# Performance work log

Hardware: AMD Instinct MI355X
Metric: run time of the kernel (lower is better)

## Reference

```python
import jax, jax.numpy as jnp
import numpy as np

B, S, D, H = 4, 2048, 1024, 16
DK = D // H
NEG = -1e9  # stand-in for -inf; keeps softmax grads NaN-free, same math after softmax


def setup_inputs() -> dict:
    key = jax.random.key(0)
    ks = jax.random.split(key, 8)
    scale = 0.02
    return {
        "q": jax.random.normal(ks[0], (B, S, D), jnp.float32),
        "k": jax.random.normal(ks[1], (B, S, D), jnp.float32),
        "v": jax.random.normal(ks[2], (B, S, D), jnp.float32),
        "mask": jnp.ones((B, S), jnp.int32),
        "Wq": jax.random.normal(ks[3], (D, D), jnp.float32) * scale,
        "bq": jnp.zeros((D,), jnp.float32),
        "Wk": jax.random.normal(ks[4], (D, D), jnp.float32) * scale,
        "bk": jnp.zeros((D,), jnp.float32),
        "Wv": jax.random.normal(ks[5], (D, D), jnp.float32) * scale,
        "bv": jnp.zeros((D,), jnp.float32),
        "Wp": jax.random.normal(ks[6], (D, D), jnp.float32) * scale,
        "bp": jnp.zeros((D,), jnp.float32),
    }


def reference(q, k, v, mask, Wq, bq, Wk, bk, Wv, bv, Wp, bp):
    # torch.nn.Linear: y = x @ W.T + b
    Q = q @ Wq.T + bq  # [B,S,D]
    K = k @ Wk.T + bk
    V = v @ Wv.T + bv
    # split heads -> [B,H,S,dk]
    Q = Q.reshape(B, S, H, DK).transpose(0, 2, 1, 3)
    K = K.reshape(B, S, H, DK).transpose(0, 2, 1, 3)
    V = V.reshape(B, S, H, DK).transpose(0, 2, 1, 3)
    Sc = jnp.einsum("bhqd,bhkd->bhqk", Q, K) / jnp.sqrt(jnp.float32(DK))
    # padding mask: [B,1,1,Sk]
    Sc = jnp.where(mask[:, None, None, :] == 0, NEG, Sc)
    # causal mask (tril), as in the registered buffer
    causal = jnp.tril(jnp.ones((S, S), jnp.bool_))
    Sc = jnp.where(causal, Sc, NEG)
    A = jax.nn.softmax(Sc, axis=-1)  # attn_drop with p=0 is identity
    x = jnp.einsum("bhqk,bhkd->bhqd", A, V)
    x = x.transpose(0, 2, 1, 3).reshape(B, S, D)
    return x @ Wp.T + bp
```

## Files before the change

### kernel.cpp

```cpp
#include <hip/hip_runtime.h>
#include <stdint.h>


#define SZB (8192u * 1024u * 2u)
#define WSZ (1024u * 1024u * 2u)
#define NKT 16
#define SLOT 24576

typedef __attribute__((ext_vector_type(8))) short  short8;
typedef __attribute__((ext_vector_type(4))) float  f32x4;

#define MFMA16(a, b, c) __builtin_amdgcn_mfma_f32_16x16x32_bf16(a, b, c, 0, 0, 0)

__device__ __forceinline__ ushort f2bf(float f) {
  uint32_t u = __float_as_uint(f);
  u += 0x7FFF + ((u >> 16) & 1);
  return (ushort)(u >> 16);
}
__device__ __forceinline__ short8 cvt8(float4 a, float4 b) {
  short8 r;
  r[0] = (short)f2bf(a.x); r[1] = (short)f2bf(a.y);
  r[2] = (short)f2bf(a.z); r[3] = (short)f2bf(a.w);
  r[4] = (short)f2bf(b.x); r[5] = (short)f2bf(b.y);
  r[6] = (short)f2bf(b.z); r[7] = (short)f2bf(b.w);
  return r;
}
__device__ __forceinline__ void gl_lds16(const ushort* g, ushort* l) {
  __builtin_amdgcn_global_load_lds(
      (__attribute__((address_space(1))) void*)g,
      (__attribute__((address_space(3))) void*)l, 16, 0, 0);
}

__global__ __launch_bounds__(256) void cvt_w(
    const float* __restrict__ Wq, const float* __restrict__ Wk,
    const float* __restrict__ Wv, const float* __restrict__ Wp,
    ushort* __restrict__ Wqb, ushort* __restrict__ Wkb,
    ushort* __restrict__ Wvb, ushort* __restrict__ Wpb) {
  const int z = blockIdx.y;
  const float* s = (z == 0) ? Wq : (z == 1) ? Wk : (z == 2) ? Wv : Wp;
  ushort* d = (z == 0) ? Wqb : (z == 1) ? Wkb : (z == 2) ? Wvb : Wpb;
  const size_t i = (size_t)(blockIdx.x * 256 + threadIdx.x) * 8;
  *(short8*)&d[i] = cvt8(*(const float4*)&s[i], *(const float4*)&s[i + 4]);
}

__global__ __launch_bounds__(256) void cvt_in(
    const float* __restrict__ q, const float* __restrict__ k,
    const float* __restrict__ v,
    ushort* __restrict__ qb2, ushort* __restrict__ kb2,
    ushort* __restrict__ vb2) {
  const int z = blockIdx.y;
  const float* s = (z == 0) ? q : (z == 1) ? k : v;
  ushort* d = (z == 0) ? qb2 : (z == 1) ? kb2 : vb2;
  const size_t i = (size_t)(blockIdx.x * 256 + threadIdx.x) * 8;
  *(short8*)&d[i] = cvt8(*(const float4*)&s[i], *(const float4*)&s[i + 4]);
}

__device__ __forceinline__ void core8p(
    const ushort* __restrict__ A, const ushort* __restrict__ Wb,
    ushort* lds, int m0, int n0, f32x4 acc[4][4]) {
  const int tid  = threadIdx.x;
  const int w    = tid >> 6;
  const int lane = tid & 63;
  const int quad = lane >> 4;
  const int l16  = lane & 15;
  const int wm   = (w >> 1) * 64;
  const int wn   = (w & 1) * 64;

  const ushort* asrc[4];
  const ushort* bsrc[2];
#pragma unroll
  for (int i = 0; i < 4; ++i) {
    const int c = tid + 512 * i;
    asrc[i] = A + (size_t)(m0 + (c >> 3)) * 1024 + ((c & 7) ^ ((c >> 3) & 7)) * 8;
  }
#pragma unroll
  for (int i = 0; i < 2; ++i) {
    const int c = tid + 512 * i;
    bsrc[i] = Wb + (size_t)(n0 + (c >> 3)) * 1024 + ((c & 7) ^ ((c >> 3) & 7)) * 8;
  }

  auto stage = [&](int j, int s) {
    ushort* base = lds + s * SLOT + w * 512;
#pragma unroll
    for (int i = 0; i < 4; ++i)
      gl_lds16(asrc[i] + j * 64, base + i * 4096);
#pragma unroll
    for (int i = 0; i < 2; ++i)
      gl_lds16(bsrc[i] + j * 64, base + 16384 + i * 4096);
  };

  const int rsw = (l16 & 7) * 8;
  auto compute = [&](int s) {
    const ushort* pA = lds + s * SLOT;
    const ushort* pB = pA + 16384;
    short8 a[4][2], b[4][2];
#pragma unroll
    for (int f = 0; f < 4; ++f)
#pragma unroll
      for (int ks = 0; ks < 2; ++ks) {
        a[f][ks] = *(const short8*)&pA[(wm + f * 16 + l16) * 64 +
                                       ((ks * 32 + quad * 8) ^ rsw)];
        b[f][ks] = *(const short8*)&pB[(wn + f * 16 + l16) * 64 +
                                       ((ks * 32 + quad * 8) ^ rsw)];
      }
    __builtin_amdgcn_s_setprio(1);
#pragma unroll
    for (int i = 0; i < 4; ++i)
#pragma unroll
      for (int j2 = 0; j2 < 4; ++j2) {
        acc[i][j2] = MFMA16(a[i][0], b[j2][0], acc[i][j2]);
        acc[i][j2] = MFMA16(a[i][1], b[j2][1], acc[i][j2]);
      }
    __builtin_amdgcn_s_setprio(0);
  };

  stage(0, 0);
  stage(1, 1);
  int s = 0;
#pragma unroll 1
  for (int j = 0; j < NKT - 1; ++j) {
    asm volatile("s_waitcnt vmcnt(6)" ::: "memory");
    __builtin_amdgcn_s_barrier();
    __builtin_amdgcn_sched_barrier(0);
    if (j < NKT - 2) {
      int s2 = s + 2; if (s2 >= 3) s2 -= 3;
      stage(j + 2, s2);
    }
    compute(s);
    if (++s == 3) s = 0;
  }
  asm volatile("s_waitcnt vmcnt(0)" ::: "memory");
  __builtin_amdgcn_s_barrier();
  __builtin_amdgcn_sched_barrier(0);
  compute(s);
}

__global__ __launch_bounds__(512, 2) void gemm_qkv8(
    const ushort* __restrict__ qb2, const ushort* __restrict__ kb2,
    const ushort* __restrict__ vb2,
    const ushort* __restrict__ Wqb, const ushort* __restrict__ Wkb,
    const ushort* __restrict__ Wvb,
    const float* __restrict__ bq, const float* __restrict__ bk,
    const float* __restrict__ bv,
    ushort* __restrict__ Qb, ushort* __restrict__ Kb, ushort* __restrict__ Vt) {
  __shared__ ushort lds[3 * SLOT];

  const int z = blockIdx.z;
  const ushort* A    = (z == 0) ? qb2 : (z == 1) ? kb2 : vb2;
  const ushort* W    = (z == 0) ? Wqb : (z == 1) ? Wkb : Wvb;
  const float*  bias = (z == 0) ? bq  : (z == 1) ? bk  : bv;

  const int m0 = blockIdx.x * 256;
  const int n0 = blockIdx.y * 128;

  f32x4 acc[4][4] = {};
  core8p(A, W, lds, m0, n0, acc);

  const int tid  = threadIdx.x;
  const int w    = tid >> 6;
  const int lane = tid & 63;
  const int quad = lane >> 4;
  const int l16  = lane & 15;
  const int wm   = (w >> 1) * 64;
  const int wn   = (w & 1) * 64;

  float bvv[4];
#pragma unroll
  for (int j = 0; j < 4; ++j) bvv[j] = bias[n0 + wn + j * 16 + l16];

  if (z < 2) {
    ushort* Out = (z == 0) ? Qb : Kb;
    const float sc = (z == 0) ? 0.1803368801f : 1.0f;
#pragma unroll
    for (int i = 0; i < 4; ++i) {
      const int m = m0 + wm + i * 16 + quad * 4;
#pragma unroll
      for (int j = 0; j < 4; ++j) {
        const int n = n0 + wn + j * 16 + l16;
#pragma unroll
        for (int r = 0; r < 4; ++r)
          Out[(size_t)(m + r) * 1024 + n] = f2bf((acc[i][j][r] + bvv[j]) * sc);
      }
    }
  } else {
#pragma unroll
    for (int i = 0; i < 4; ++i) {
      const int mrow = m0 + wm + i * 16 + quad * 4;
      const int bb   = mrow >> 11;
      const int s0   = mrow & 2047;
#pragma unroll
      for (int j = 0; j < 4; ++j) {
        const int n = n0 + wn + j * 16 + l16;
        ushort4 pk;
        pk.x = f2bf(acc[i][j][0] + bvv[j]);
        pk.y = f2bf(acc[i][j][1] + bvv[j]);
        pk.z = f2bf(acc[i][j][2] + bvv[j]);
        pk.w = f2bf(acc[i][j][3] + bvv[j]);
        *(ushort4*)&Vt[(size_t)((bb * 16 + (n >> 6)) * 64 + (n & 63)) * 2048 + s0] = pk;
      }
    }
  }
}

__global__ __launch_bounds__(512, 2) void gemm_proj8(
    const ushort* __restrict__ Xin, const ushort* __restrict__ Wpb,
    const float* __restrict__ bp, float* __restrict__ Out) {
  __shared__ ushort lds[3 * SLOT];

  const int m0 = blockIdx.x * 256;
  const int n0 = blockIdx.y * 128;

  f32x4 acc[4][4] = {};
  core8p(Xin, Wpb, lds, m0, n0, acc);

  const int tid  = threadIdx.x;
  const int w    = tid >> 6;
  const int lane = tid & 63;
  const int quad = lane >> 4;
  const int l16  = lane & 15;
  const int wm   = (w >> 1) * 64;
  const int wn   = (w & 1) * 64;

  float bvv[4];
#pragma unroll
  for (int j = 0; j < 4; ++j) bvv[j] = bp[n0 + wn + j * 16 + l16];

#pragma unroll
  for (int i = 0; i < 4; ++i) {
    const int m = m0 + wm + i * 16 + quad * 4;
#pragma unroll
    for (int j = 0; j < 4; ++j) {
      const int n = n0 + wn + j * 16 + l16;
#pragma unroll
      for (int r = 0; r < 4; ++r)
        Out[(size_t)(m + r) * 1024 + n] = acc[i][j][r] + bvv[j];
    }
  }
}

__global__ __launch_bounds__(256) void gemm_v_fb(
    const float* __restrict__ vin, const ushort* __restrict__ Wvb,
    const float* __restrict__ bv, ushort* __restrict__ Vt) {
  __shared__ ushort As[128 * 32];
  __shared__ ushort Bs[128 * 32];

  const int tid  = threadIdx.x;
  const int w    = tid >> 6;
  const int lane = tid & 63;
  const int quad = lane >> 4;
  const int l16  = lane & 15;
  const int wm   = (w >> 1) * 64;
  const int wn   = (w & 1) * 64;
  const int r0   = tid >> 2;
  const int r1   = r0 + 64;
  const int c0   = (tid & 3) * 8;

  const int m0 = blockIdx.x * 128;
  const int n0 = blockIdx.y * 128;

  f32x4 acc[4][4] = {};
  const ushort* Wg = Wvb + (size_t)(n0 + w * 32 + (lane >> 2)) * 1024 + (lane & 3) * 8;
  const float*  Ag0 = vin + (size_t)(m0 + r0) * 1024 + c0;
  const float*  Ag1 = vin + (size_t)(m0 + r1) * 1024 + c0;

  float4 p0a = *(const float4*)(Ag0), p0b = *(const float4*)(Ag0 + 4);
  float4 p1a = *(const float4*)(Ag1), p1b = *(const float4*)(Ag1 + 4);

  for (int kt = 0; kt < 32; ++kt) {
    const int ko = kt * 32;
    __syncthreads();
    *(short8*)&As[r0 * 32 + c0] = cvt8(p0a, p0b);
    *(short8*)&As[r1 * 32 + c0] = cvt8(p1a, p1b);
    gl_lds16(Wg + ko,         &Bs[(w * 32) * 32]);
    gl_lds16(Wg + 16384 + ko, &Bs[(w * 32 + 16) * 32]);
    __syncthreads();
    if (kt < 31) {
      const int kn = ko + 32;
      p0a = *(const float4*)(Ag0 + kn); p0b = *(const float4*)(Ag0 + kn + 4);
      p1a = *(const float4*)(Ag1 + kn); p1b = *(const float4*)(Ag1 + kn + 4);
    }
    short8 af[4], bfr[4];
#pragma unroll
    for (int i = 0; i < 4; ++i)
      af[i] = *(const short8*)&As[(wm + i * 16 + l16) * 32 + quad * 8];
#pragma unroll
    for (int i = 0; i < 4; ++i)
      bfr[i] = *(const short8*)&Bs[(wn + i * 16 + l16) * 32 + quad * 8];
#pragma unroll
    for (int i = 0; i < 4; ++i)
#pragma unroll
      for (int j = 0; j < 4; ++j)
        acc[i][j] = MFMA16(af[i], bfr[j], acc[i][j]);
  }

  float bvv[4];
#pragma unroll
  for (int j = 0; j < 4; ++j) bvv[j] = bv[n0 + wn + j * 16 + l16];
#pragma unroll
  for (int i = 0; i < 4; ++i) {
    const int mrow = m0 + wm + i * 16 + quad * 4;
    const int bb   = mrow >> 11;
    const int s0   = mrow & 2047;
#pragma unroll
    for (int j = 0; j < 4; ++j) {
      const int n = n0 + wn + j * 16 + l16;
      ushort4 pk;
      pk.x = f2bf(acc[i][j][0] + bvv[j]);
      pk.y = f2bf(acc[i][j][1] + bvv[j]);
      pk.z = f2bf(acc[i][j][2] + bvv[j]);
      pk.w = f2bf(acc[i][j][3] + bvv[j]);
      *(ushort4*)&Vt[(size_t)((bb * 16 + (n >> 6)) * 64 + (n & 63)) * 2048 + s0] = pk;
    }
  }
}

__global__ __launch_bounds__(256, 4) void attn(
    ushort* __restrict__ Qb, const ushort* __restrict__ Kb,
    const ushort* __restrict__ Vt, const int* __restrict__ mask) {
  __shared__ ushort Ks[64 * 68];
  __shared__ ushort Vts[64 * 68];
  __shared__ ushort Ps[4][16 * 68];

  const int wgid = (int)blockIdx.x + 16 * (int)blockIdx.y;
  const int xcd  = wgid & 7;
  const int idx  = wgid >> 3;
  const int bh   = xcd * 8 + (idx >> 4);
  const int pair = idx & 15;
  const int b = bh >> 4, h = bh & 15;
  const int tid = threadIdx.x, w = tid >> 6, lane = tid & 63;
  const int quad = lane >> 4, l16 = lane & 15;

  short8 kst[2], vst[2];
  int pmn[4];

  auto ld_tile = [&](int k0) {
#pragma unroll
    for (int i = 0; i < 2; ++i) {
      const int c = tid + 256 * i;
      kst[i] = *(const short8*)&Kb[(size_t)(b * 2048 + k0 + (c >> 3)) * 1024 +
                                   h * 64 + (c & 7) * 8];
      vst[i] = *(const short8*)&Vt[(size_t)(bh * 64 + (c >> 3)) * 2048 +
                                   k0 + (c & 7) * 8];
    }
#pragma unroll
    for (int nj = 0; nj < 4; ++nj) pmn[nj] = mask[b * 2048 + k0 + nj * 16 + l16];
  };

#pragma unroll 1
  for (int seg = 0; seg < 2; ++seg) {
    const int qt = seg ? (31 - pair) : pair;
    const int q0 = qt * 64;

    const size_t qoff = (size_t)(b * 2048 + q0 + w * 16 + l16) * 1024 + h * 64 + quad * 8;
    const short8 qf0 = *(const short8*)&Qb[qoff];
    const short8 qf1 = *(const short8*)&Qb[qoff + 32];

    f32x4 oacc[4] = {};
    float lsum[4] = {0.f, 0.f, 0.f, 0.f};

    ld_tile(0);

    for (int kt = 0; kt <= qt; ++kt) {
      __syncthreads();
#pragma unroll
      for (int i = 0; i < 2; ++i) {
        const int c = tid + 256 * i;
        *(short8*)&Ks[(c >> 3) * 68 + (c & 7) * 8]  = kst[i];
        *(short8*)&Vts[(c >> 3) * 68 + (c & 7) * 8] = vst[i];
      }
      int pmc[4];
#pragma unroll
      for (int nj = 0; nj < 4; ++nj) pmc[nj] = pmn[nj];
      __syncthreads();

      if (kt < qt) ld_tile((kt + 1) * 64);

      f32x4 sc[4];
#pragma unroll
      for (int nj = 0; nj < 4; ++nj) {
        f32x4 z4 = {0.f, 0.f, 0.f, 0.f};
        const short8 kf0 = *(const short8*)&Ks[(nj * 16 + l16) * 68 + quad * 8];
        const short8 kf1 = *(const short8*)&Ks[(nj * 16 + l16) * 68 + 32 + quad * 8];
        z4 = MFMA16(qf0, kf0, z4);
        z4 = MFMA16(qf1, kf1, z4);
        sc[nj] = z4;
      }

      if (kt < qt) {
#pragma unroll
        for (int nj = 0; nj < 4; ++nj)
#pragma unroll
          for (int r = 0; r < 4; ++r) {
            const float e = (pmc[nj] != 0) ? sc[nj][r] : -1e5f;
            const float p = __builtin_amdgcn_exp2f(e);
            lsum[r] += p;
            Ps[w][(quad * 4 + r) * 68 + nj * 16 + l16] = f2bf(p);
          }
      } else {
        const int k0 = kt * 64;
#pragma unroll
        for (int nj = 0; nj < 4; ++nj) {
          const int key = k0 + nj * 16 + l16;
#pragma unroll
          for (int r = 0; r < 4; ++r) {
            const int qr = q0 + w * 16 + quad * 4 + r;
            const bool ok = (pmc[nj] != 0) && (key <= qr);
            const float e = ok ? sc[nj][r] : -1e5f;
            const float p = __builtin_amdgcn_exp2f(e);
            lsum[r] += p;
            Ps[w][(quad * 4 + r) * 68 + nj * 16 + l16] = f2bf(p);
          }
        }
      }

#pragma unroll
      for (int ks = 0; ks < 2; ++ks) {
        const short8 pf = *(const short8*)&Ps[w][l16 * 68 + ks * 32 + quad * 8];
#pragma unroll
        for (int nb = 0; nb < 4; ++nb) {
          const short8 vf = *(const short8*)&Vts[(nb * 16 + l16) * 68 + ks * 32 + quad * 8];
          oacc[nb] = MFMA16(pf, vf, oacc[nb]);
        }
      }
    }

#pragma unroll
    for (int r = 0; r < 4; ++r) {
      float v = lsum[r];
      v += __shfl_xor(v, 1);
      v += __shfl_xor(v, 2);
      v += __shfl_xor(v, 4);
      v += __shfl_xor(v, 8);
      lsum[r] = 1.0f / v;
    }
#pragma unroll
    for (int nb = 0; nb < 4; ++nb)
#pragma unroll
      for (int r = 0; r < 4; ++r) {
        const int q = q0 + w * 16 + quad * 4 + r;
        Qb[(size_t)(b * 2048 + q) * 1024 + h * 64 + nb * 16 + l16] =
            f2bf(oacc[nb][r] * lsum[r]);
      }
  }
}

extern "C" void kernel_launch(void* const* d_in, const int* in_sizes, int n_in,
                              void* d_out, int out_size, void* d_ws, size_t ws_size,
                              hipStream_t stream) {
  const float* q    = (const float*)d_in[0];
  const float* k    = (const float*)d_in[1];
  const float* v    = (const float*)d_in[2];
  const int*   mask = (const int*)d_in[3];
  const float* Wq   = (const float*)d_in[4];
  const float* bq   = (const float*)d_in[5];
  const float* Wk   = (const float*)d_in[6];
  const float* bk   = (const float*)d_in[7];
  const float* Wv   = (const float*)d_in[8];
  const float* bv   = (const float*)d_in[9];
  const float* Wp   = (const float*)d_in[10];
  const float* bp   = (const float*)d_in[11];
  float* out = (float*)d_out;

  char* ws = (char*)d_ws;
  ushort* Qb  = (ushort*)(ws);
  ushort* Kb  = (ushort*)(ws + (size_t)SZB);
  ushort* Vt  = (ushort*)(ws + (size_t)2 * SZB);
  ushort* Wqb = (ushort*)(ws + (size_t)3 * SZB);
  ushort* Wkb = (ushort*)(ws + (size_t)3 * SZB + WSZ);
  ushort* Wvb = (ushort*)(ws + (size_t)3 * SZB + 2 * WSZ);
  ushort* Wpb = (ushort*)(ws + (size_t)3 * SZB + 3 * WSZ);

  ushort* qb2 = (ushort*)out;
  ushort* kb2 = (ushort*)((char*)out + (size_t)SZB);
  const size_t need_v = (size_t)3 * SZB + 4 * WSZ + SZB;
  const int v_bf = (ws_size >= need_v) ? 1 : 0;
  ushort* vb2 = v_bf ? (ushort*)(ws + (size_t)3 * SZB + 4 * WSZ) : nullptr;

  cvt_w<<<dim3(512, 4), dim3(256), 0, stream>>>(Wq, Wk, Wv, Wp, Wqb, Wkb, Wvb, Wpb);
  cvt_in<<<dim3(4096, 2 + v_bf), dim3(256), 0, stream>>>(q, k, v, qb2, kb2, vb2);
  gemm_qkv8<<<dim3(32, 8, 2 + v_bf), dim3(512), 0, stream>>>(
      qb2, kb2, vb2, Wqb, Wkb, Wvb, bq, bk, bv, Qb, Kb, Vt);
  if (!v_bf)
    gemm_v_fb<<<dim3(64, 8), dim3(256), 0, stream>>>(v, Wvb, bv, Vt);
  attn<<<dim3(16, 64), dim3(256), 0, stream>>>(Qb, Kb, Vt, mask);
  gemm_proj8<<<dim3(32, 8), dim3(512), 0, stream>>>(Qb, Wpb, bp, out);
}
```

Baseline: 327.2 us.

## Keep softmax probabilities in registers via transposed QK MFMA and K16 PV

The score MFMA now has its operands swapped, so each lane holds S^T fragments whose layout matches the A operand of a 16x16x16 bf16 MFMA. This lets P feed directly into the PV product without the per-wave LDS round trip through Ps. The mask is loaded once per lane and turned into a wave ballot, with a fast path when every key in the tile is valid. Hardware packed bf16 conversion replaces the manual rounding. The trade-off is twice as many, smaller MFMAs for PV, plus a reworked row-sum reduction and shuffle at the end.

```diff
diff --git a/kernel.cpp b/kernel.cpp
--- a/kernel.cpp
+++ b/kernel.cpp
@@ -8,9 +8,25 @@
 #define SLOT 24576
 
 typedef __attribute__((ext_vector_type(8))) short  short8;
+typedef __attribute__((ext_vector_type(4))) short  short4v;
 typedef __attribute__((ext_vector_type(4))) float  f32x4;
 
 #define MFMA16(a, b, c) __builtin_amdgcn_mfma_f32_16x16x32_bf16(a, b, c, 0, 0, 0)
+
+__device__ __forceinline__ f32x4 mfma_k16(short4v a, short4v b, f32x4 c) {
+#if __has_builtin(__builtin_amdgcn_mfma_f32_16x16x16bf16_1k)
+  return __builtin_amdgcn_mfma_f32_16x16x16bf16_1k(a, b, c, 0, 0, 0);
+#else
+  asm volatile("v_mfma_f32_16x16x16_bf16 %0, %1, %2, %0"
+               : "+v"(c) : "v"(a), "v"(b));
+  return c;
+#endif
+}
+__device__ __forceinline__ uint32_t cvtpk(float a, float b) {
+  uint32_t r;
+  asm("v_cvt_pk_bf16_f32 %0, %1, %2" : "=v"(r) : "v"(a), "v"(b));
+  return r;
+}
 
 __device__ __forceinline__ ushort f2bf(float f) {
   uint32_t u = __float_as_uint(f);
@@ -319,7 +335,6 @@
     const ushort* __restrict__ Vt, const int* __restrict__ mask) {
   __shared__ ushort Ks[64 * 68];
   __shared__ ushort Vts[64 * 68];
-  __shared__ ushort Ps[4][16 * 68];
 
   const int wgid = (int)blockIdx.x + 16 * (int)blockIdx.y;
   const int xcd  = wgid & 7;
@@ -329,9 +344,10 @@
   const int b = bh >> 4, h = bh & 15;
   const int tid = threadIdx.x, w = tid >> 6, lane = tid & 63;
   const int quad = lane >> 4, l16 = lane & 15;
+  const int ql = w * 16 + l16;
 
   short8 kst[2], vst[2];
-  int pmn[4];
+  int mld;
 
   auto ld_tile = [&](int k0) {
 #pragma unroll
@@ -342,8 +358,7 @@
       vst[i] = *(const short8*)&Vt[(size_t)(bh * 64 + (c >> 3)) * 2048 +
                                    k0 + (c & 7) * 8];
     }
-#pragma unroll
-    for (int nj = 0; nj < 4; ++nj) pmn[nj] = mask[b * 2048 + k0 + nj * 16 + l16];
+    mld = mask[b * 2048 + k0 + lane];
   };
 
 #pragma unroll 1
@@ -368,12 +383,13 @@
         *(short8*)&Ks[(c >> 3) * 68 + (c & 7) * 8]  = kst[i];
         *(short8*)&Vts[(c >> 3) * 68 + (c & 7) * 8] = vst[i];
       }
-      int pmc[4];
-#pragma unroll
-      for (int nj = 0; nj < 4; ++nj) pmc[nj] = pmn[nj];
+      const int mcur = mld;
       __syncthreads();
 
       if (kt < qt) ld_tile((kt + 1) * 64);
+
+      const unsigned long long mbits = __ballot(mcur != 0);
+      const bool allm = (mbits == ~0ull);
 
       f32x4 sc[4];
 #pragma unroll
@@ -381,65 +397,81 @@
         f32x4 z4 = {0.f, 0.f, 0.f, 0.f};
         const short8 kf0 = *(const short8*)&Ks[(nj * 16 + l16) * 68 + quad * 8];
         const short8 kf1 = *(const short8*)&Ks[(nj * 16 + l16) * 68 + 32 + quad * 8];
-        z4 = MFMA16(qf0, kf0, z4);
-        z4 = MFMA16(qf1, kf1, z4);
+        z4 = MFMA16(kf0, qf0, z4);
+        z4 = MFMA16(kf1, qf1, z4);
         sc[nj] = z4;
       }
 
+      float pv[4][4];
       if (kt < qt) {
-#pragma unroll
-        for (int nj = 0; nj < 4; ++nj)
-#pragma unroll
-          for (int r = 0; r < 4; ++r) {
-            const float e = (pmc[nj] != 0) ? sc[nj][r] : -1e5f;
-            const float p = __builtin_amdgcn_exp2f(e);
-            lsum[r] += p;
-            Ps[w][(quad * 4 + r) * 68 + nj * 16 + l16] = f2bf(p);
-          }
-      } else {
-        const int k0 = kt * 64;
-#pragma unroll
-        for (int nj = 0; nj < 4; ++nj) {
-          const int key = k0 + nj * 16 + l16;
-#pragma unroll
-          for (int r = 0; r < 4; ++r) {
-            const int qr = q0 + w * 16 + quad * 4 + r;
-            const bool ok = (pmc[nj] != 0) && (key <= qr);
-            const float e = ok ? sc[nj][r] : -1e5f;
-            const float p = __builtin_amdgcn_exp2f(e);
-            lsum[r] += p;
-            Ps[w][(quad * 4 + r) * 68 + nj * 16 + l16] = f2bf(p);
+        if (allm) {
+#pragma unroll
+          for (int nj = 0; nj < 4; ++nj)
+#pragma unroll
+            for (int r = 0; r < 4; ++r)
+              pv[nj][r] = __builtin_amdgcn_exp2f(sc[nj][r]);
+        } else {
+#pragma unroll
+          for (int nj = 0; nj < 4; ++nj) {
+            const uint32_t sub = (uint32_t)(mbits >> (nj * 16));
+#pragma unroll
+            for (int r = 0; r < 4; ++r) {
+              const bool ok = (sub >> (quad * 4 + r)) & 1;
+              pv[nj][r] = __builtin_amdgcn_exp2f(ok ? sc[nj][r] : -1e5f);
+            }
           }
         }
-      }
-
-#pragma unroll
-      for (int ks = 0; ks < 2; ++ks) {
-        const short8 pf = *(const short8*)&Ps[w][l16 * 68 + ks * 32 + quad * 8];
+      } else {
+#pragma unroll
+        for (int nj = 0; nj < 4; ++nj) {
+          const uint32_t sub = allm ? 0xffffffffu : (uint32_t)(mbits >> (nj * 16));
+#pragma unroll
+          for (int r = 0; r < 4; ++r) {
+            const int kl = nj * 16 + quad * 4 + r;
+            const bool ok = ((sub >> (quad * 4 + r)) & 1) && (kl <= ql);
+            pv[nj][r] = __builtin_amdgcn_exp2f(ok ? sc[nj][r] : -1e5f);
+          }
+        }
+      }
+#pragma unroll
+      for (int nj = 0; nj < 4; ++nj)
+#pragma unroll
+        for (int r = 0; r < 4; ++r) lsum[r] += pv[nj][r];
+
+      short4v pa[4];
+#pragma unroll
+      for (int nj = 0; nj < 4; ++nj) {
+        uint32_t u0 = cvtpk(pv[nj][0], pv[nj][1]);
+        uint32_t u1 = cvtpk(pv[nj][2], pv[nj][3]);
+        pa[nj][0] = (short)(u0 & 0xffff); pa[nj][1] = (short)(u0 >> 16);
+        pa[nj][2] = (short)(u1 & 0xffff); pa[nj][3] = (short)(u1 >> 16);
+      }
+
+#pragma unroll
+      for (int nj = 0; nj < 4; ++nj)
 #pragma unroll
         for (int nb = 0; nb < 4; ++nb) {
-          const short8 vf = *(const short8*)&Vts[(nb * 16 + l16) * 68 + ks * 32 + quad * 8];
-          oacc[nb] = MFMA16(pf, vf, oacc[nb]);
+          const short4v vf = *(const short4v*)&Vts[(nb * 16 + l16) * 68 +
+                                                   nj * 16 + quad * 4];
+          oacc[nb] = mfma_k16(pa[nj], vf, oacc[nb]);
         }
-      }
-    }
-
-#pragma unroll
-    for (int r = 0; r < 4; ++r) {
-      float v = lsum[r];
-      v += __shfl_xor(v, 1);
-      v += __shfl_xor(v, 2);
-      v += __shfl_xor(v, 4);
-      v += __shfl_xor(v, 8);
-      lsum[r] = 1.0f / v;
-    }
+    }
+
+    float v = lsum[0] + lsum[1] + lsum[2] + lsum[3];
+    v += __shfl_xor(v, 16);
+    v += __shfl_xor(v, 32);
+    const float inv = 1.0f / v;
+    float invr[4];
+#pragma unroll
+    for (int r = 0; r < 4; ++r) invr[r] = __shfl(inv, quad * 4 + r);
+
 #pragma unroll
     for (int nb = 0; nb < 4; ++nb)
 #pragma unroll
       for (int r = 0; r < 4; ++r) {
         const int q = q0 + w * 16 + quad * 4 + r;
         Qb[(size_t)(b * 2048 + q) * 1024 + h * 64 + nb * 16 + l16] =
-            f2bf(oacc[nb][r] * lsum[r]);
+            f2bf(oacc[nb][r] * invr[r]);
       }
   }
 }
```

Result: faster. 311.2 us (-4.9%).
